# Performance work log

Hardware: AMD Instinct MI355X
Metric: run time of the kernel (lower is better)

## Reference

```python
import jax, jax.numpy as jnp
import numpy as np

B, T, C = 8, 2048, 256
H = 4
HD = C // H  # 64

def setup_inputs() -> dict:
    key = jax.random.key(0)
    ks = jax.random.split(key, 5)
    s = 1.0 / np.sqrt(C)
    return {
        "x": jax.random.normal(ks[0], (B, T, C), dtype=jnp.float32),
        "w_qkv": jax.random.uniform(ks[1], (3 * C, C), jnp.float32, -s, s),
        "b_qkv": jax.random.uniform(ks[2], (3 * C,), jnp.float32, -s, s),
        "w_proj": jax.random.uniform(ks[3], (C, C), jnp.float32, -s, s),
        "b_proj": jax.random.uniform(ks[4], (C,), jnp.float32, -s, s),
    }

def reference(x, w_qkv, b_qkv, w_proj, b_proj):
    # qkv projection: [B,T,3C] -> [3,B,H,T,HD]
    qkv = x @ w_qkv.T + b_qkv
    qkv = qkv.reshape(B, T, 3, H, HD).transpose(2, 0, 3, 1, 4)
    q, k, v = qkv[0], qkv[1], qkv[2]
    scale = HD ** -0.5
    attn = jnp.einsum("bhqd,bhkd->bhqk", q, k) * scale
    attn = jax.nn.softmax(attn, axis=-1)  # dropout is identity in eval
    out = jnp.einsum("bhqk,bhkd->bhqd", attn, v)
    out = out.transpose(0, 2, 1, 3).reshape(B, T, C)
    return out @ w_proj.T + b_proj
```

## Files before the change

### kernel.cpp

```cpp
#include <hip/hip_runtime.h>
#include <hip/hip_bf16.h>
#include <cstdint>
#include <cstddef>


typedef __attribute__((ext_vector_type(8))) __bf16 bf16x8;
typedef __attribute__((ext_vector_type(4))) float f32x4;
typedef __attribute__((ext_vector_type(16))) float f32x16;

__device__ __forceinline__ f32x4 mfma16(bf16x8 a, bf16x8 b, f32x4 c) {
  return __builtin_amdgcn_mfma_f32_16x16x32_bf16(a, b, c, 0, 0, 0);
}
__device__ __forceinline__ f32x16 mfma32(bf16x8 a, bf16x8 b, f32x16 c) {
  return __builtin_amdgcn_mfma_f32_32x32x16_bf16(a, b, c, 0, 0, 0);
}

__device__ __forceinline__ void gload_lds16(const __bf16* g, __bf16* l) {
  __builtin_amdgcn_global_load_lds(
      (const __attribute__((address_space(1))) void*)g,
      (__attribute__((address_space(3))) void*)l, 16, 0, 0);
}

__device__ __forceinline__ uint32_t cvtpk_bf16(float lo, float hi) {
  uint32_t r;
  asm("v_cvt_pk_bf16_f32 %0, %1, %2" : "=v"(r) : "v"(lo), "v"(hi));
  return r;
}

__global__ __launch_bounds__(256) void cast_all(
    const float* __restrict__ x, const float* __restrict__ wq,
    const float* __restrict__ wp,
    __bf16* __restrict__ xb, __bf16* __restrict__ wqb, __bf16* __restrict__ wpb) {
  const int NX = (16384 * 256) / 4, NQ = (768 * 256) / 4, NP = (256 * 256) / 4;
  int i = blockIdx.x * 256 + threadIdx.x;
  const float4* src;
  __bf16* dst;
  int j;
  if (i < NX) { src = (const float4*)x; dst = xb; j = i; }
  else if (i < NX + NQ) { src = (const float4*)wq; dst = wqb; j = i - NX; }
  else if (i < NX + NQ + NP) { src = (const float4*)wp; dst = wpb; j = i - NX - NQ; }
  else return;
  float4 v = src[j];
  union { __bf16 b[4]; ushort4 u; } o;
  o.b[0] = (__bf16)v.x; o.b[1] = (__bf16)v.y; o.b[2] = (__bf16)v.z; o.b[3] = (__bf16)v.w;
  ((ushort4*)dst)[j] = o.u;
}

template <int EPI>
__global__ __launch_bounds__(256) void gemm_nt(
    const __bf16* __restrict__ A, const __bf16* __restrict__ B,
    const float* __restrict__ bias, int K, int N,
    __bf16* __restrict__ qo, __bf16* __restrict__ ko, __bf16* __restrict__ vo,
    float* __restrict__ fo) {
  const int tid = threadIdx.x;
  const int lane = tid & 63;
  const int w = tid >> 6;
  const int wr = w >> 1, wc = w & 1;
  const int m0 = blockIdx.x * 128, n0 = blockIdx.y * 128;
  const int l15 = lane & 15, lhi = lane >> 4;
  const bool vswap = (EPI == 0) && (n0 >= 512);

  __shared__ __align__(16) __bf16 As[128 * 64];
  __shared__ __align__(16) __bf16 Bs[128 * 64];

  const f32x4 fzero = {0.f, 0.f, 0.f, 0.f};
  f32x4 acc[4][4];
#pragma unroll
  for (int i = 0; i < 4; i++)
#pragma unroll
    for (int j = 0; j < 4; j++) acc[i][j] = fzero;

  for (int k0 = 0; k0 < K; k0 += 64) {
#pragma unroll
    for (int it = 0; it < 4; ++it) {
      int c = it * 256 + tid;
      int row = c >> 3, cc = c & 7;
      int col = ((cc ^ (row & 7)) << 3);
      gload_lds16(A + (size_t)(m0 + row) * K + k0 + col, As + c * 8);
      gload_lds16(B + (size_t)(n0 + row) * K + k0 + col, Bs + c * 8);
    }
    asm volatile("s_waitcnt vmcnt(0)" ::: "memory");
    __syncthreads();

    bf16x8 af[4][2], bfr[4][2];
#pragma unroll
    for (int i = 0; i < 4; i++)
#pragma unroll
      for (int kk = 0; kk < 2; kk++) {
        af[i][kk]  = *(const bf16x8*)(
            As + (wr * 64 + i * 16 + l15) * 64 + (((kk * 4 + lhi) ^ (l15 & 7)) << 3));
        bfr[i][kk] = *(const bf16x8*)(
            Bs + (wc * 64 + i * 16 + l15) * 64 + (((kk * 4 + lhi) ^ (l15 & 7)) << 3));
      }
    __builtin_amdgcn_s_setprio(1);
    if (!vswap) {
#pragma unroll
      for (int kk = 0; kk < 2; kk++)
#pragma unroll
        for (int mi = 0; mi < 4; mi++)
#pragma unroll
          for (int ni = 0; ni < 4; ni++)
            acc[mi][ni] = mfma16(af[mi][kk], bfr[ni][kk], acc[mi][ni]);
    } else {
#pragma unroll
      for (int kk = 0; kk < 2; kk++)
#pragma unroll
        for (int mi = 0; mi < 4; mi++)
#pragma unroll
          for (int ni = 0; ni < 4; ni++)
            acc[mi][ni] = mfma16(bfr[ni][kk], af[mi][kk], acc[mi][ni]);
    }
    __builtin_amdgcn_s_setprio(0);
    __syncthreads();
  }

  if (vswap) {
#pragma unroll
    for (int mi = 0; mi < 4; mi++) {
#pragma unroll
      for (int ni = 0; ni < 4; ni++) {
        int tg = m0 + wr * 64 + mi * 16 + l15;
        int nb = n0 + wc * 64 + ni * 16 + (lhi << 2);
        int b = tg >> 11, t = tg & 2047;
#pragma unroll
        for (int r = 0; r < 4; r++) {
          int n = nb + r;
          float val = acc[mi][ni][r] + bias[n];
          int hd = n - 512;
          int h = hd >> 6, d = hd & 63;
          vo[((size_t)(b * 4 + h) * 64 + d) * 2048 + t] = (__bf16)val;
        }
      }
    }
    return;
  }

#pragma unroll
  for (int mi = 0; mi < 4; mi++) {
#pragma unroll
    for (int ni = 0; ni < 4; ni++) {
      int col = n0 + wc * 64 + ni * 16 + l15;
      int rowb = m0 + wr * 64 + mi * 16 + (lhi << 2);
      float bv = bias[col];
#pragma unroll
      for (int r = 0; r < 4; r++) {
        float val = acc[mi][ni][r] + bv;
        int rr = rowb + r;
        if (EPI == 0) {
          int h = (col >> 6) & 3;
          int d = col & 63;
          int b = rr >> 11;
          int t = rr & 2047;
          size_t bh = (size_t)(b * 4 + h);
          if (col < 256) {
            qo[(bh * 2048 + t) * 64 + d] = (__bf16)(val * 0.18033688f);
          } else {
            ko[(bh * 2048 + t) * 64 + d] = (__bf16)val;
          }
        } else {
          fo[(size_t)rr * N + col] = val;
        }
      }
    }
  }
}

__global__ __launch_bounds__(256, 2) void attn_kernel(
    const __bf16* __restrict__ Q, const __bf16* __restrict__ Kb,
    const __bf16* __restrict__ Vt, __bf16* __restrict__ Ao) {
  const int tid = threadIdx.x, lane = tid & 63, w = tid >> 6;
  const int l31 = lane & 31, hi = lane >> 5;
  const int bh = blockIdx.x;
  const int q0 = blockIdx.y * 128;
  const int b = bh >> 2, h = bh & 3;

  __shared__ __align__(16) __bf16 Ks[2][64 * 64];
  __shared__ __align__(16) __bf16 Vs[2][64 * 64];
  __shared__ float Ls[4][32];

  const __bf16* Qb = Q + (size_t)bh * 2048 * 64;
  const __bf16* Kbase = Kb + (size_t)bh * 2048 * 64;
  const __bf16* Vbase = Vt + (size_t)bh * 64 * 2048;

  const int qrow = q0 + w * 32 + l31;
  bf16x8 qf[4];
#pragma unroll
  for (int dc = 0; dc < 4; dc++)
    qf[dc] = *(const bf16x8*)(Qb + (size_t)qrow * 64 + dc * 16 + hi * 8);

  f32x16 oacc[2];
#pragma unroll
  for (int i = 0; i < 16; i++) { oacc[0][i] = 0.f; oacc[1][i] = 0.f; }
  float lrun = 0.f;

  const int r0 = tid >> 3, p0c = tid & 7;
  const int s0 = ((p0c ^ (r0 & 7)) << 3);
  const int r1 = (tid + 256) >> 3, p1c = tid & 7;
  const int s1 = ((p1c ^ (r1 & 7)) << 3);

  gload_lds16(Kbase + (size_t)r0 * 64 + s0, &Ks[0][tid * 8]);
  gload_lds16(Kbase + (size_t)r1 * 64 + s1, &Ks[0][(tid + 256) * 8]);
  gload_lds16(Vbase + (size_t)r0 * 2048 + s0, &Vs[0][tid * 8]);
  gload_lds16(Vbase + (size_t)r1 * 2048 + s1, &Vs[0][(tid + 256) * 8]);

  int cur = 0;
  const int swz = (l31 & 7);

  for (int kt = 0; kt < 32; ++kt) {
    __syncthreads();

    if (kt + 1 < 32) {
      const __bf16* Kg = Kbase + (size_t)(kt + 1) * 64 * 64;
      const __bf16* Vg = Vbase + (size_t)(kt + 1) * 64;
      gload_lds16(Kg + (size_t)r0 * 64 + s0, &Ks[cur ^ 1][tid * 8]);
      gload_lds16(Kg + (size_t)r1 * 64 + s1, &Ks[cur ^ 1][(tid + 256) * 8]);
      gload_lds16(Vg + (size_t)r0 * 2048 + s0, &Vs[cur ^ 1][tid * 8]);
      gload_lds16(Vg + (size_t)r1 * 2048 + s1, &Vs[cur ^ 1][(tid + 256) * 8]);
    }

    const __bf16* Kl = &Ks[cur][0];
    const __bf16* Vl = &Vs[cur][0];

    f32x16 sacc[2];
#pragma unroll
    for (int i = 0; i < 16; i++) { sacc[0][i] = -16.f; sacc[1][i] = -16.f; }
#pragma unroll
    for (int kb = 0; kb < 2; kb++) {
      bf16x8 kf[4];
#pragma unroll
      for (int dc = 0; dc < 4; dc++)
        kf[dc] = *(const bf16x8*)(
            Kl + (kb * 32 + l31) * 64 + (((dc * 2 + hi) ^ swz) << 3));
      __builtin_amdgcn_s_setprio(1);
#pragma unroll
      for (int dc = 0; dc < 4; dc++)
        sacc[kb] = mfma32(kf[dc], qf[dc], sacc[kb]);
      __builtin_amdgcn_s_setprio(0);
    }

#pragma unroll
    for (int kb = 0; kb < 2; kb++)
#pragma unroll
      for (int i = 0; i < 16; i++) sacc[kb][i] = exp2f(sacc[kb][i]);

    uint32_t wo[8][2];
#pragma unroll
    for (int kb = 0; kb < 2; kb++)
#pragma unroll
      for (int e = 0; e < 4; e++) {
        wo[kb * 4 + e][0] = cvtpk_bf16(sacc[kb][4 * e + 0], sacc[kb][4 * e + 1]);
        wo[kb * 4 + e][1] = cvtpk_bf16(sacc[kb][4 * e + 2], sacc[kb][4 * e + 3]);
      }
    bf16x8 pa[4];
#pragma unroll
    for (int ks = 0; ks < 4; ks++) {
      uint32_t a0 = wo[2 * ks][0], b0 = wo[2 * ks + 1][0];
      uint32_t a1 = wo[2 * ks][1], b1 = wo[2 * ks + 1][1];
      asm("v_permlane32_swap_b32 %0, %1" : "+v"(a0), "+v"(b0));
      asm("v_permlane32_swap_b32 %0, %1" : "+v"(a1), "+v"(b1));
      union { uint32_t u[4]; bf16x8 v; } f;
      f.u[0] = a0; f.u[1] = a1; f.u[2] = b0; f.u[3] = b1;
      pa[ks] = f.v;
    }

    float red[16];
#pragma unroll
    for (int i = 0; i < 16; i++) red[i] = sacc[0][i] + sacc[1][i];
#pragma unroll
    for (int s = 8; s >= 1; s >>= 1)
#pragma unroll
      for (int i = 0; i < 8; i++)
        if (i < s) red[i] += red[i + s];
    lrun += red[0] + __shfl_xor(red[0], 32);

#pragma unroll
    for (int db = 0; db < 2; db++) {
      bf16x8 vf[4];
#pragma unroll
      for (int ks = 0; ks < 4; ks++)
        vf[ks] = *(const bf16x8*)(
            Vl + (db * 32 + l31) * 64 + (((ks * 2 + hi) ^ swz) << 3));
      __builtin_amdgcn_s_setprio(1);
#pragma unroll
      for (int ks = 0; ks < 4; ks++)
        oacc[db] = mfma32(pa[ks], vf[ks], oacc[db]);
      __builtin_amdgcn_s_setprio(0);
    }

    cur ^= 1;
  }

  if (hi == 0) Ls[w][l31] = lrun;
  asm volatile("s_waitcnt lgkmcnt(0)" ::: "memory");
  __builtin_amdgcn_sched_barrier(0);
  float linv[16];
#pragma unroll
  for (int r = 0; r < 16; r++)
    linv[r] = 1.0f / Ls[w][4 * hi + (r & 3) + 8 * (r >> 2)];
#pragma unroll
  for (int db = 0; db < 2; db++)
#pragma unroll
    for (int r = 0; r < 16; r++) {
      int qr = 4 * hi + (r & 3) + 8 * (r >> 2);
      int t = q0 + w * 32 + qr;
      Ao[((size_t)(b * 2048 + t)) * 256 + h * 64 + db * 32 + l31] =
          (__bf16)(oacc[db][r] * linv[r]);
    }
}

extern "C" void kernel_launch(void* const* d_in, const int* in_sizes, int n_in,
                              void* d_out, int out_size, void* d_ws, size_t ws_size,
                              hipStream_t stream) {
  const float* x      = (const float*)d_in[0];
  const float* w_qkv  = (const float*)d_in[1];
  const float* b_qkv  = (const float*)d_in[2];
  const float* w_proj = (const float*)d_in[3];
  const float* b_proj = (const float*)d_in[4];
  float* out = (float*)d_out;

  char* ws = (char*)d_ws;
  __bf16* xb  = (__bf16*)ws; ws += (size_t)16384 * 256 * 2;
  __bf16* wqb = (__bf16*)ws; ws += (size_t)768 * 256 * 2;
  __bf16* wpb = (__bf16*)ws; ws += (size_t)256 * 256 * 2;
  __bf16* qb  = (__bf16*)ws; ws += (size_t)8 * 4 * 2048 * 64 * 2;
  __bf16* kb  = (__bf16*)ws; ws += (size_t)8 * 4 * 2048 * 64 * 2;
  __bf16* vb  = (__bf16*)ws; ws += (size_t)8 * 4 * 2048 * 64 * 2;
  __bf16* aob = (__bf16*)ws; ws += (size_t)16384 * 256 * 2;

  int castN = (16384 * 256 + 768 * 256 + 256 * 256) / 4;
  cast_all<<<(castN + 255) / 256, 256, 0, stream>>>(x, w_qkv, w_proj, xb, wqb, wpb);
  gemm_nt<0><<<dim3(128, 6), 256, 0, stream>>>(xb, wqb, b_qkv, 256, 768,
                                               qb, kb, vb, nullptr);
  attn_kernel<<<dim3(32, 16), 256, 0, stream>>>(qb, kb, vb, aob);
  gemm_nt<1><<<dim3(128, 2), 256, 0, stream>>>(aob, wpb, b_proj, 256, 256,
                                               nullptr, nullptr, nullptr, out);
}
```

Before: 160.6 us.

## Fuse x cast into QKV GEMM and double attention KV tile to 128

The separate fp32-to-bf16 cast of x is removed: the QKV GEMM now streams fp32 x tiles into LDS and converts to bf16 while building MFMA fragments. This drops a full read and write of the activation tensor and part of a kernel's work. The attention kernel now loads 128-key K/V tiles per double-buffer stage, halving loop iterations and barriers. In exchange it doubles LDS use, which may reduce occupancy, and the GEMM A tile doubles in LDS size and adds conversion work.

```diff
diff --git a/kernel.cpp b/kernel.cpp
--- a/kernel.cpp
+++ b/kernel.cpp
@@ -15,7 +15,7 @@
   return __builtin_amdgcn_mfma_f32_32x32x16_bf16(a, b, c, 0, 0, 0);
 }
 
-__device__ __forceinline__ void gload_lds16(const __bf16* g, __bf16* l) {
+__device__ __forceinline__ void gload_lds16(const void* g, void* l) {
   __builtin_amdgcn_global_load_lds(
       (const __attribute__((address_space(1))) void*)g,
       (__attribute__((address_space(3))) void*)l, 16, 0, 0);
@@ -27,18 +27,16 @@
   return r;
 }
 
-__global__ __launch_bounds__(256) void cast_all(
-    const float* __restrict__ x, const float* __restrict__ wq,
-    const float* __restrict__ wp,
-    __bf16* __restrict__ xb, __bf16* __restrict__ wqb, __bf16* __restrict__ wpb) {
-  const int NX = (16384 * 256) / 4, NQ = (768 * 256) / 4, NP = (256 * 256) / 4;
+__global__ __launch_bounds__(256) void cast_w(
+    const float* __restrict__ wq, const float* __restrict__ wp,
+    __bf16* __restrict__ wqb, __bf16* __restrict__ wpb) {
+  const int NQ = (768 * 256) / 4, NP = (256 * 256) / 4;
   int i = blockIdx.x * 256 + threadIdx.x;
   const float4* src;
   __bf16* dst;
   int j;
-  if (i < NX) { src = (const float4*)x; dst = xb; j = i; }
-  else if (i < NX + NQ) { src = (const float4*)wq; dst = wqb; j = i - NX; }
-  else if (i < NX + NQ + NP) { src = (const float4*)wp; dst = wpb; j = i - NX - NQ; }
+  if (i < NQ) { src = (const float4*)wq; dst = wqb; j = i; }
+  else if (i < NQ + NP) { src = (const float4*)wp; dst = wpb; j = i - NQ; }
   else return;
   float4 v = src[j];
   union { __bf16 b[4]; ushort4 u; } o;
@@ -48,7 +46,7 @@
 
 template <int EPI>
 __global__ __launch_bounds__(256) void gemm_nt(
-    const __bf16* __restrict__ A, const __bf16* __restrict__ B,
+    const void* __restrict__ Av, const __bf16* __restrict__ B,
     const float* __restrict__ bias, int K, int N,
     __bf16* __restrict__ qo, __bf16* __restrict__ ko, __bf16* __restrict__ vo,
     float* __restrict__ fo) {
@@ -60,7 +58,11 @@
   const int l15 = lane & 15, lhi = lane >> 4;
   const bool vswap = (EPI == 0) && (n0 >= 512);
 
-  __shared__ __align__(16) __bf16 As[128 * 64];
+  const float* Af = (const float*)Av;
+  const __bf16* Ab = (const __bf16*)Av;
+
+  __shared__ __align__(16) float  Asf[EPI == 0 ? 128 * 64 : 4];
+  __shared__ __align__(16) __bf16 Asb[EPI == 1 ? 128 * 64 : 8];
   __shared__ __align__(16) __bf16 Bs[128 * 64];
 
   const f32x4 fzero = {0.f, 0.f, 0.f, 0.f};
@@ -71,12 +73,29 @@
     for (int j = 0; j < 4; j++) acc[i][j] = fzero;
 
   for (int k0 = 0; k0 < K; k0 += 64) {
-#pragma unroll
-    for (int it = 0; it < 4; ++it) {
-      int c = it * 256 + tid;
+    if constexpr (EPI == 0) {
+#pragma unroll
+      for (int t = 0; t < 8; ++t) {
+        int c = t * 256 + tid;
+        int row = c >> 4, cc = c & 15;
+        int p = cc >> 1, lo = cc & 1;
+        int colf = ((((p ^ (row & 7)) << 1) | lo) << 2);
+        gload_lds16(Af + (size_t)(m0 + row) * K + k0 + colf, Asf + c * 4);
+      }
+    } else {
+#pragma unroll
+      for (int t = 0; t < 4; ++t) {
+        int c = t * 256 + tid;
+        int row = c >> 3, cc = c & 7;
+        int col = ((cc ^ (row & 7)) << 3);
+        gload_lds16(Ab + (size_t)(m0 + row) * K + k0 + col, Asb + c * 8);
+      }
+    }
+#pragma unroll
+    for (int t = 0; t < 4; ++t) {
+      int c = t * 256 + tid;
       int row = c >> 3, cc = c & 7;
       int col = ((cc ^ (row & 7)) << 3);
-      gload_lds16(A + (size_t)(m0 + row) * K + k0 + col, As + c * 8);
       gload_lds16(B + (size_t)(n0 + row) * K + k0 + col, Bs + c * 8);
     }
     asm volatile("s_waitcnt vmcnt(0)" ::: "memory");
@@ -87,8 +106,22 @@
     for (int i = 0; i < 4; i++)
 #pragma unroll
       for (int kk = 0; kk < 2; kk++) {
-        af[i][kk]  = *(const bf16x8*)(
-            As + (wr * 64 + i * 16 + l15) * 64 + (((kk * 4 + lhi) ^ (l15 & 7)) << 3));
+        int row = wr * 64 + i * 16 + l15;
+        if constexpr (EPI == 0) {
+          const float* src =
+              Asf + row * 64 + (((kk * 4 + lhi) ^ (l15 & 7)) << 3);
+          float4 fa = *(const float4*)src;
+          float4 fb = *(const float4*)(src + 4);
+          union { uint32_t u[4]; bf16x8 v; } t;
+          t.u[0] = cvtpk_bf16(fa.x, fa.y);
+          t.u[1] = cvtpk_bf16(fa.z, fa.w);
+          t.u[2] = cvtpk_bf16(fb.x, fb.y);
+          t.u[3] = cvtpk_bf16(fb.z, fb.w);
+          af[i][kk] = t.v;
+        } else {
+          af[i][kk] = *(const bf16x8*)(
+              Asb + row * 64 + (((kk * 4 + lhi) ^ (l15 & 7)) << 3));
+        }
         bfr[i][kk] = *(const bf16x8*)(
             Bs + (wc * 64 + i * 16 + l15) * 64 + (((kk * 4 + lhi) ^ (l15 & 7)) << 3));
       }
@@ -174,8 +207,8 @@
   const int q0 = blockIdx.y * 128;
   const int b = bh >> 2, h = bh & 3;
 
-  __shared__ __align__(16) __bf16 Ks[2][64 * 64];
-  __shared__ __align__(16) __bf16 Vs[2][64 * 64];
+  __shared__ __align__(16) __bf16 Ks[2][128 * 64];
+  __shared__ __align__(16) __bf16 Vs[2][64 * 128];
   __shared__ float Ls[4][32];
 
   const __bf16* Qb = Q + (size_t)bh * 2048 * 64;
@@ -193,98 +226,112 @@
   for (int i = 0; i < 16; i++) { oacc[0][i] = 0.f; oacc[1][i] = 0.f; }
   float lrun = 0.f;
 
-  const int r0 = tid >> 3, p0c = tid & 7;
-  const int s0 = ((p0c ^ (r0 & 7)) << 3);
-  const int r1 = (tid + 256) >> 3, p1c = tid & 7;
-  const int s1 = ((p1c ^ (r1 & 7)) << 3);
-
-  gload_lds16(Kbase + (size_t)r0 * 64 + s0, &Ks[0][tid * 8]);
-  gload_lds16(Kbase + (size_t)r1 * 64 + s1, &Ks[0][(tid + 256) * 8]);
-  gload_lds16(Vbase + (size_t)r0 * 2048 + s0, &Vs[0][tid * 8]);
-  gload_lds16(Vbase + (size_t)r1 * 2048 + s1, &Vs[0][(tid + 256) * 8]);
+  int kr[4], kc[4], vr[4], vc[4];
+#pragma unroll
+  for (int t = 0; t < 4; ++t) {
+    int c = t * 256 + tid;
+    kr[t] = c >> 3;
+    kc[t] = (((c & 7) ^ (kr[t] & 7)) << 3);
+    vr[t] = c >> 4;
+    vc[t] = ((((c & 15) & 8) | (((c & 15) & 7) ^ (vr[t] & 7))) << 3);
+  }
+
+  {
+#pragma unroll
+    for (int t = 0; t < 4; ++t) {
+      int c = t * 256 + tid;
+      gload_lds16(Kbase + (size_t)kr[t] * 64 + kc[t], &Ks[0][c * 8]);
+      gload_lds16(Vbase + (size_t)vr[t] * 2048 + vc[t], &Vs[0][c * 8]);
+    }
+  }
 
   int cur = 0;
   const int swz = (l31 & 7);
 
-  for (int kt = 0; kt < 32; ++kt) {
+  for (int kt = 0; kt < 16; ++kt) {
     __syncthreads();
 
-    if (kt + 1 < 32) {
-      const __bf16* Kg = Kbase + (size_t)(kt + 1) * 64 * 64;
-      const __bf16* Vg = Vbase + (size_t)(kt + 1) * 64;
-      gload_lds16(Kg + (size_t)r0 * 64 + s0, &Ks[cur ^ 1][tid * 8]);
-      gload_lds16(Kg + (size_t)r1 * 64 + s1, &Ks[cur ^ 1][(tid + 256) * 8]);
-      gload_lds16(Vg + (size_t)r0 * 2048 + s0, &Vs[cur ^ 1][tid * 8]);
-      gload_lds16(Vg + (size_t)r1 * 2048 + s1, &Vs[cur ^ 1][(tid + 256) * 8]);
-    }
-
-    const __bf16* Kl = &Ks[cur][0];
-    const __bf16* Vl = &Vs[cur][0];
-
-    f32x16 sacc[2];
-#pragma unroll
-    for (int i = 0; i < 16; i++) { sacc[0][i] = -16.f; sacc[1][i] = -16.f; }
-#pragma unroll
-    for (int kb = 0; kb < 2; kb++) {
-      bf16x8 kf[4];
-#pragma unroll
-      for (int dc = 0; dc < 4; dc++)
-        kf[dc] = *(const bf16x8*)(
-            Kl + (kb * 32 + l31) * 64 + (((dc * 2 + hi) ^ swz) << 3));
-      __builtin_amdgcn_s_setprio(1);
-#pragma unroll
-      for (int dc = 0; dc < 4; dc++)
-        sacc[kb] = mfma32(kf[dc], qf[dc], sacc[kb]);
-      __builtin_amdgcn_s_setprio(0);
-    }
-
-#pragma unroll
-    for (int kb = 0; kb < 2; kb++)
-#pragma unroll
-      for (int i = 0; i < 16; i++) sacc[kb][i] = exp2f(sacc[kb][i]);
-
-    uint32_t wo[8][2];
-#pragma unroll
-    for (int kb = 0; kb < 2; kb++)
-#pragma unroll
-      for (int e = 0; e < 4; e++) {
-        wo[kb * 4 + e][0] = cvtpk_bf16(sacc[kb][4 * e + 0], sacc[kb][4 * e + 1]);
-        wo[kb * 4 + e][1] = cvtpk_bf16(sacc[kb][4 * e + 2], sacc[kb][4 * e + 3]);
-      }
-    bf16x8 pa[4];
-#pragma unroll
-    for (int ks = 0; ks < 4; ks++) {
-      uint32_t a0 = wo[2 * ks][0], b0 = wo[2 * ks + 1][0];
-      uint32_t a1 = wo[2 * ks][1], b1 = wo[2 * ks + 1][1];
-      asm("v_permlane32_swap_b32 %0, %1" : "+v"(a0), "+v"(b0));
-      asm("v_permlane32_swap_b32 %0, %1" : "+v"(a1), "+v"(b1));
-      union { uint32_t u[4]; bf16x8 v; } f;
-      f.u[0] = a0; f.u[1] = a1; f.u[2] = b0; f.u[3] = b1;
-      pa[ks] = f.v;
-    }
-
-    float red[16];
-#pragma unroll
-    for (int i = 0; i < 16; i++) red[i] = sacc[0][i] + sacc[1][i];
-#pragma unroll
-    for (int s = 8; s >= 1; s >>= 1)
-#pragma unroll
-      for (int i = 0; i < 8; i++)
-        if (i < s) red[i] += red[i + s];
-    lrun += red[0] + __shfl_xor(red[0], 32);
-
-#pragma unroll
-    for (int db = 0; db < 2; db++) {
-      bf16x8 vf[4];
-#pragma unroll
-      for (int ks = 0; ks < 4; ks++)
-        vf[ks] = *(const bf16x8*)(
-            Vl + (db * 32 + l31) * 64 + (((ks * 2 + hi) ^ swz) << 3));
-      __builtin_amdgcn_s_setprio(1);
-#pragma unroll
-      for (int ks = 0; ks < 4; ks++)
-        oacc[db] = mfma32(pa[ks], vf[ks], oacc[db]);
-      __builtin_amdgcn_s_setprio(0);
+    if (kt + 1 < 16) {
+      const __bf16* Kg = Kbase + (size_t)(kt + 1) * 128 * 64;
+      const __bf16* Vg = Vbase + (size_t)(kt + 1) * 128;
+#pragma unroll
+      for (int t = 0; t < 4; ++t) {
+        int c = t * 256 + tid;
+        gload_lds16(Kg + (size_t)kr[t] * 64 + kc[t], &Ks[cur ^ 1][c * 8]);
+        gload_lds16(Vg + (size_t)vr[t] * 2048 + vc[t], &Vs[cur ^ 1][c * 8]);
+      }
+    }
+
+#pragma unroll
+    for (int hf = 0; hf < 2; ++hf) {
+      const __bf16* Kl = &Ks[cur][hf * 64 * 64];
+      const __bf16* Vl = &Vs[cur][hf * 64];
+
+      f32x16 sacc[2];
+#pragma unroll
+      for (int i = 0; i < 16; i++) { sacc[0][i] = -16.f; sacc[1][i] = -16.f; }
+#pragma unroll
+      for (int kb = 0; kb < 2; kb++) {
+        bf16x8 kf[4];
+#pragma unroll
+        for (int dc = 0; dc < 4; dc++)
+          kf[dc] = *(const bf16x8*)(
+              Kl + (kb * 32 + l31) * 64 + (((dc * 2 + hi) ^ swz) << 3));
+        __builtin_amdgcn_s_setprio(1);
+#pragma unroll
+        for (int dc = 0; dc < 4; dc++)
+          sacc[kb] = mfma32(kf[dc], qf[dc], sacc[kb]);
+        __builtin_amdgcn_s_setprio(0);
+      }
+
+#pragma unroll
+      for (int kb = 0; kb < 2; kb++)
+#pragma unroll
+        for (int i = 0; i < 16; i++) sacc[kb][i] = exp2f(sacc[kb][i]);
+
+      uint32_t wo[8][2];
+#pragma unroll
+      for (int kb = 0; kb < 2; kb++)
+#pragma unroll
+        for (int e = 0; e < 4; e++) {
+          wo[kb * 4 + e][0] = cvtpk_bf16(sacc[kb][4 * e + 0], sacc[kb][4 * e + 1]);
+          wo[kb * 4 + e][1] = cvtpk_bf16(sacc[kb][4 * e + 2], sacc[kb][4 * e + 3]);
+        }
+      bf16x8 pa[4];
+#pragma unroll
+      for (int ks = 0; ks < 4; ks++) {
+        uint32_t a0 = wo[2 * ks][0], b0 = wo[2 * ks + 1][0];
+        uint32_t a1 = wo[2 * ks][1], b1 = wo[2 * ks + 1][1];
+        asm("v_permlane32_swap_b32 %0, %1" : "+v"(a0), "+v"(b0));
+        asm("v_permlane32_swap_b32 %0, %1" : "+v"(a1), "+v"(b1));
+        union { uint32_t u[4]; bf16x8 v; } f;
+        f.u[0] = a0; f.u[1] = a1; f.u[2] = b0; f.u[3] = b1;
+        pa[ks] = f.v;
+      }
+
+      float red[16];
+#pragma unroll
+      for (int i = 0; i < 16; i++) red[i] = sacc[0][i] + sacc[1][i];
+#pragma unroll
+      for (int s = 8; s >= 1; s >>= 1)
+#pragma unroll
+        for (int i = 0; i < 8; i++)
+          if (i < s) red[i] += red[i + s];
+      lrun += red[0] + __shfl_xor(red[0], 32);
+
+#pragma unroll
+      for (int db = 0; db < 2; db++) {
+        bf16x8 vf[4];
+#pragma unroll
+        for (int ks = 0; ks < 4; ks++)
+          vf[ks] = *(const bf16x8*)(
+              Vl + (db * 32 + l31) * 128 + (((ks * 2 + hi) ^ swz) << 3));
+        __builtin_amdgcn_s_setprio(1);
+#pragma unroll
+        for (int ks = 0; ks < 4; ks++)
+          oacc[db] = mfma32(pa[ks], vf[ks], oacc[db]);
+        __builtin_amdgcn_s_setprio(0);
+      }
     }
 
     cur ^= 1;
@@ -319,7 +366,6 @@
   float* out = (float*)d_out;
 
   char* ws = (char*)d_ws;
-  __bf16* xb  = (__bf16*)ws; ws += (size_t)16384 * 256 * 2;
   __bf16* wqb = (__bf16*)ws; ws += (size_t)768 * 256 * 2;
   __bf16* wpb = (__bf16*)ws; ws += (size_t)256 * 256 * 2;
   __bf16* qb  = (__bf16*)ws; ws += (size_t)8 * 4 * 2048 * 64 * 2;
@@ -327,9 +373,9 @@
   __bf16* vb  = (__bf16*)ws; ws += (size_t)8 * 4 * 2048 * 64 * 2;
   __bf16* aob = (__bf16*)ws; ws += (size_t)16384 * 256 * 2;
 
-  int castN = (16384 * 256 + 768 * 256 + 256 * 256) / 4;
-  cast_all<<<(castN + 255) / 256, 256, 0, stream>>>(x, w_qkv, w_proj, xb, wqb, wpb);
-  gemm_nt<0><<<dim3(128, 6), 256, 0, stream>>>(xb, wqb, b_qkv, 256, 768,
+  int castN = (768 * 256 + 256 * 256) / 4;
+  cast_w<<<(castN + 255) / 256, 256, 0, stream>>>(w_qkv, w_proj, wqb, wpb);
+  gemm_nt<0><<<dim3(128, 6), 256, 0, stream>>>(x, wqb, b_qkv, 256, 768,
                                                qb, kb, vb, nullptr);
   attn_kernel<<<dim3(32, 16), 256, 0, stream>>>(qb, kb, vb, aob);
   gemm_nt<1><<<dim3(128, 2), 256, 0, stream>>>(aob, wpb, b_proj, 256, 256,
```

Measured after the change: 168.0 us. +4.6%, slower.
